# Performance work log

Hardware: AMD Instinct MI355X
Metric: run time of the kernel (lower is better)

Reference implementation:

```python
import jax, jax.numpy as jnp
import numpy as np

B, T, E, H = 4, 2048, 1024, 16
HS = E // H  # head_size = 64


def setup_inputs() -> dict:
    key = jax.random.key(0)
    ks = jax.random.split(key, 5)
    x = jax.random.normal(ks[0], (B, T, E), jnp.float32)
    scale = 0.02
    Wq = jax.random.normal(ks[1], (H, E, HS), jnp.float32) * scale
    Wk = jax.random.normal(ks[2], (H, E, HS), jnp.float32) * scale
    Wv = jax.random.normal(ks[3], (H, E, HS), jnp.float32) * scale
    Wo = jax.random.normal(ks[4], (E, E), jnp.float32) * scale
    bo = jnp.zeros((E,), jnp.float32)
    return {"x": x, "Wq": Wq, "Wk": Wk, "Wv": Wv, "Wo": Wo, "bo": bo}


def reference(x, Wq, Wk, Wv, Wo, bo):
    b, t, e = x.shape
    # per-head projections, batched over heads
    Q = jnp.einsum('bte,hed->bhtd', x, Wq)  # (B,H,T,HS)
    K = jnp.einsum('bte,hed->bhtd', x, Wk)
    V = jnp.einsum('bte,hed->bhtd', x, Wv)
    # faithful quirk 1: scale by sqrt(embd_size), not sqrt(head_size)
    scores = jnp.einsum('bhtd,bhsd->bhts', Q, K) / jnp.sqrt(jnp.float32(e))
    mask = jnp.tril(jnp.ones((t, t), dtype=bool))  # (T_q, T_k)
    scores = jnp.where(mask[None, None, :, :], scores, -jnp.inf)
    # faithful quirk 2: original softmaxes over dim=1 of (B,Tq,Tk) = the QUERY axis
    attn = jax.nn.softmax(scores, axis=2)
    out = jnp.einsum('bhts,bhsd->bhtd', attn, V)  # (B,H,T,HS)
    out = out.transpose(0, 2, 1, 3).reshape(b, t, e)  # concat heads -> (B,T,E)
    return out @ Wo + bo
```

## Files before the change

kernel.cpp:

```cpp
#include <hip/hip_runtime.h>
#include <stdint.h>

#define Bn 4
#define Tn 2048
#define En 1024
#define Hn 16
#define HSn 64
#define BHn (Bn*Hn)
#define NRn (Bn*Tn)

#define CEXP 0.0450840831f

typedef __attribute__((ext_vector_type(8))) short short8;
typedef __attribute__((ext_vector_type(4))) float f32x4;
typedef __attribute__((ext_vector_type(16))) float f32x16;
typedef __attribute__((ext_vector_type(4))) unsigned int uint4w;

__device__ __forceinline__ unsigned short f2b(float f){
  union { float f; unsigned int u; } c; c.f = f;
  unsigned int u = c.u + 0x7FFFu + ((c.u >> 16) & 1u);
  return (unsigned short)(u >> 16);
}
__device__ __forceinline__ float b2f(unsigned short s){
  union { unsigned int u; float f; } c; c.u = ((unsigned int)s) << 16;
  return c.f;
}
__device__ __forceinline__ unsigned int cvtpk(float lo, float hi){
  unsigned int r;
  asm("v_cvt_pk_bf16_f32 %0, %1, %2" : "=v"(r) : "v"(lo), "v"(hi));
  return r;
}
__device__ __forceinline__ f32x4 mfma16(short8 a, short8 b, f32x4 c){
  return __builtin_amdgcn_mfma_f32_16x16x32_bf16(a, b, c, 0, 0, 0);
}
__device__ __forceinline__ f32x16 mfma32(short8 a, short8 b, f32x16 c){
  return __builtin_amdgcn_mfma_f32_32x32x16_bf16(a, b, c, 0, 0, 0);
}
__device__ __forceinline__ void gl16(const void* g, void* s){
  __builtin_amdgcn_global_load_lds((const __attribute__((address_space(1))) unsigned int*)g,
                                   (__attribute__((address_space(3))) unsigned int*)s, 16, 0, 0);
}

__global__ void k_cvt_x(const float* __restrict__ x, unsigned short* __restrict__ xb){
  int i = (blockIdx.x * blockDim.x + threadIdx.x) * 8;
  float4 a = *(const float4*)(x + i);
  float4 b = *(const float4*)(x + i + 4);
  alignas(16) unsigned short o[8] = {f2b(a.x),f2b(a.y),f2b(a.z),f2b(a.w),
                                     f2b(b.x),f2b(b.y),f2b(b.z),f2b(b.w)};
  *(uint4w*)(xb + i) = *(const uint4w*)o;
}

__global__ void k_wT(const float* __restrict__ Wq, const float* __restrict__ Wk,
                     const float* __restrict__ Wv, const float* __restrict__ Wo,
                     unsigned short* __restrict__ Wt, unsigned short* __restrict__ Wot)
{
  __shared__ unsigned short Ls[64*80];
  const int tid = threadIdx.x;
  const int ey = blockIdx.x, jt = blockIdx.y;
  const int e0 = ey*64;
  const float* src; int R, c0; unsigned short* outp;
  if (jt < 48){
    int sel = jt >> 4, h = jt & 15;
    const float* W = (sel==0)?Wq:((sel==1)?Wk:Wv);
    src = W + h*(En*HSn); R = HSn; c0 = 0;
    outp = Wt + jt*64*En;
  } else {
    src = Wo; R = En; c0 = (jt-48)*64;
    outp = Wot + (jt-48)*64*En;
  }
  {
    const int e = tid >> 2, cq = (tid & 3)*16;
    const float* p = src + (e0 + e)*R + c0 + cq;
    float vv[16];
    *(float4*)&vv[0]  = *(const float4*)(p);
    *(float4*)&vv[4]  = *(const float4*)(p+4);
    *(float4*)&vv[8]  = *(const float4*)(p+8);
    *(float4*)&vv[12] = *(const float4*)(p+12);
#pragma unroll
    for (int i = 0; i < 16; i++) Ls[(cq+i)*80 + e] = f2b(vv[i]);
  }
  __syncthreads();
  {
    const int c8 = tid & 7, r = tid >> 3;
#pragma unroll
    for (int rr0 = 0; rr0 < 2; rr0++){
      int rr = r + rr0*32;
      *(uint4w*)(outp + rr*En + e0 + c8*8) = *(const uint4w*)&Ls[rr*80 + c8*8];
    }
  }
}

__global__ void __launch_bounds__(256, 2)
k_qkv(const unsigned short* __restrict__ xb,
      const unsigned short* __restrict__ Wt,
      unsigned short* __restrict__ Qb, unsigned short* __restrict__ Kb,
      unsigned short* __restrict__ Vt)
{
  __shared__ unsigned short As[2][128*64];
  __shared__ unsigned short Bs[2][128*64];
  const int tid = threadIdx.x, lane = tid & 63, w = tid >> 6;
  const int wr = w >> 1, wc = w & 1;
  const int mb = blockIdx.x, nb = blockIdx.y;
  const int n0 = nb*128;
  const int sel = n0 >> 10;
  const int nj0 = n0 & 1023;
  const int l15 = lane & 15, kc = lane >> 4;
  const int r8 = lane >> 3, c7 = lane & 7;

  const unsigned short* xbase = xb + (mb*128)*En;
  const unsigned short* wbase = Wt + n0*En;

  f32x4 acc[4][4];
#pragma unroll
  for (int i = 0; i < 4; i++)
#pragma unroll
    for (int j = 0; j < 4; j++) acc[i][j] = (f32x4){0.f,0.f,0.f,0.f};

  auto stage = [&](int buf, int k0){
#pragma unroll
    for (int i = 0; i < 4; i++){
      const int rb = w*32 + i*8;
      const int r = rb + r8;
      const int g = (c7 ^ r8) * 8;
      gl16(xbase + r*En + k0 + g, &As[buf][rb*64]);
      gl16(wbase + r*En + k0 + g, &Bs[buf][rb*64]);
    }
  };

  stage(0, 0);
  __syncthreads();

  for (int kt = 0; kt < 16; kt++){
    const int cur = kt & 1;
    if (kt < 15) stage(cur ^ 1, (kt + 1)*64);
    const unsigned short* Ac = &As[cur][0];
    const unsigned short* Bc = &Bs[cur][0];
#pragma unroll
    for (int ks = 0; ks < 2; ks++){
      short8 af[4], bf[4];
#pragma unroll
      for (int mf = 0; mf < 4; mf++){
        int ar = wr*64 + mf*16 + l15;
        af[mf] = *(const short8*)&Ac[ar*64 + (((ks*4 + kc) ^ (ar & 7))*8)];
      }
#pragma unroll
      for (int nf = 0; nf < 4; nf++){
        int br = wc*64 + nf*16 + l15;
        bf[nf] = *(const short8*)&Bc[br*64 + (((ks*4 + kc) ^ (br & 7))*8)];
      }
      __builtin_amdgcn_s_setprio(1);
#pragma unroll
      for (int mf = 0; mf < 4; mf++)
#pragma unroll
        for (int nf = 0; nf < 4; nf++)
          acc[mf][nf] = mfma16(af[mf], bf[nf], acc[mf][nf]);
      __builtin_amdgcn_s_setprio(0);
    }
    __syncthreads();
  }

  const int q4 = (lane >> 4)*4;
  const int bb = mb >> 4;
  const int tt0 = (mb*128) & 2047;

  if (sel == 2){
    unsigned short* tb = ((w < 2) ? &As[0][0] : &Bs[0][0]) + (w & 1)*8192;
#pragma unroll
    for (int nf = 0; nf < 4; nf++)
#pragma unroll
      for (int mf = 0; mf < 4; mf++){
        uint2 u;
        u.x = cvtpk(acc[mf][nf][0], acc[mf][nf][1]);
        u.y = cvtpk(acc[mf][nf][2], acc[mf][nf][3]);
        *(uint2*)&tb[(nf*16 + l15)*72 + mf*16 + q4] = u;
      }
    const int hh = (nj0 >> 6) + wc;
    unsigned short* vb = Vt + ((bb*Hn + hh)*HSn)*Tn + tt0 + wr*64;
#pragma unroll
    for (int i = 0; i < 8; i++){
      int rr = i*8 + r8;
      *(uint4w*)(vb + rr*Tn + c7*8) = *(const uint4w*)&tb[rr*72 + c7*8];
    }
  } else {
    unsigned short* Out = (sel == 1) ? Kb : Qb;
#pragma unroll
    for (int nf = 0; nf < 4; nf++){
      int jj = nj0 + wc*64 + nf*16 + l15;
      int hh = jj >> 6, dd = jj & 63;
#pragma unroll
      for (int mf = 0; mf < 4; mf++){
#pragma unroll
        for (int q = 0; q < 4; q++){
          int tt = tt0 + wr*64 + mf*16 + q4 + q;
          Out[((bb*Hn + hh)*Tn + tt)*HSn + dd] = f2b(acc[mf][nf][q]);
        }
      }
    }
  }
}

__global__ void k_colsum(const unsigned short* __restrict__ Qb,
                         const unsigned short* __restrict__ Kb,
                         float* __restrict__ Linv)
{
  __shared__ unsigned short Qs[2][128*64];
  __shared__ float Lred[64];
  const int bh = blockIdx.x, ipair = blockIdx.y;
  const int tid = threadIdx.x, lane = tid & 63, w = tid >> 6;
  const int l5 = lane >> 5, l31 = lane & 31;

  for (int ph = 0; ph < 2; ph++){
    const int sb = ph ? (31 - ipair) : ipair;
    const int s0 = sb * 64;

    short8 kf[2][4];
#pragma unroll
    for (int sf = 0; sf < 2; sf++){
      const unsigned short* kr = Kb + (bh*Tn + s0 + sf*32 + l31)*HSn + 8*l5;
#pragma unroll
      for (int ks = 0; ks < 4; ks++) kf[sf][ks] = *(const short8*)(kr + 16*ks);
    }

    float ls[2][16];
#pragma unroll
    for (int sf = 0; sf < 2; sf++)
#pragma unroll
      for (int r = 0; r < 16; r++) ls[sf][r] = 0.f;

    if (tid < 64) Lred[tid] = 0.f;

    const int t0s = (s0 >> 7) << 7;
    const int ntl = (Tn - t0s) >> 7;

    {
      const int c = lane & 7;
#pragma unroll
      for (int i = 0; i < 4; i++){
        int row = (w*4 + i)*8 + (lane >> 3);
        gl16(Qb + (bh*Tn + t0s + row)*HSn + ((c ^ (row & 7))*8), &Qs[0][(w*4 + i)*512]);
      }
    }
    asm volatile("s_waitcnt vmcnt(0)" ::: "memory");
    __syncthreads();

    for (int it = 0; it < ntl; it++){
      const int cur = it & 1;
      if (it + 1 < ntl){
        const int tn = t0s + (it + 1)*128;
        const int c = lane & 7;
#pragma unroll
        for (int i = 0; i < 4; i++){
          int row = (w*4 + i)*8 + (lane >> 3);
          gl16(Qb + (bh*Tn + tn + row)*HSn + ((c ^ (row & 7))*8), &Qs[cur^1][(w*4 + i)*512]);
        }
      }
      const int t0 = t0s + it*128;
      const int tw = t0 + 32*w;
      if (tw + 31 >= s0){
        f32x16 st[2];
#pragma unroll
        for (int sf = 0; sf < 2; sf++)
#pragma unroll
          for (int r = 0; r < 16; r++) st[sf][r] = 0.f;
        const int qrow = w*32 + l31;
        const unsigned short* Qc = &Qs[cur][qrow*64];
        const int sw = qrow & 7;
        __builtin_amdgcn_s_setprio(1);
#pragma unroll
        for (int ks = 0; ks < 4; ks++){
          short8 qb = *(const short8*)&Qc[((l5 + 2*ks) ^ sw)*8];
          st[0] = mfma32(kf[0][ks], qb, st[0]);
          st[1] = mfma32(kf[1][ks], qb, st[1]);
        }
        __builtin_amdgcn_s_setprio(0);
        const int tg = tw + l31;
        if (s0 + 63 <= tw){
#pragma unroll
          for (int sf = 0; sf < 2; sf++)
#pragma unroll
            for (int r = 0; r < 16; r++)
              ls[sf][r] += __builtin_amdgcn_exp2f(st[sf][r] * CEXP);
        } else {
#pragma unroll
          for (int sf = 0; sf < 2; sf++)
#pragma unroll
            for (int r = 0; r < 16; r++){
              int sg = s0 + 32*sf + (r & 3) + 8*(r >> 2) + 4*l5;
              float e = __builtin_amdgcn_exp2f(st[sf][r] * CEXP);
              ls[sf][r] += (tg >= sg) ? e : 0.f;
            }
        }
      }
      asm volatile("s_waitcnt vmcnt(0)" ::: "memory");
      __syncthreads();
    }

#pragma unroll
    for (int sf = 0; sf < 2; sf++)
#pragma unroll
      for (int r = 0; r < 16; r++){
        float v = ls[sf][r];
        v += __shfl_xor(v, 1);  v += __shfl_xor(v, 2);
        v += __shfl_xor(v, 4);  v += __shfl_xor(v, 8);
        v += __shfl_xor(v, 16);
        ls[sf][r] = v;
      }
    if (l31 == 0){
#pragma unroll
      for (int sf = 0; sf < 2; sf++)
#pragma unroll
        for (int r = 0; r < 16; r++){
          int sl = 32*sf + (r & 3) + 8*(r >> 2) + 4*l5;
          atomicAdd(&Lred[sl], ls[sf][r]);
        }
    }
    __syncthreads();
    if (tid < 64) Linv[bh*Tn + s0 + tid] = 1.0f / Lred[tid];
    if (ph == 0) __syncthreads();
  }
}

__global__ void k_vscale(unsigned short* __restrict__ Vt, const float* __restrict__ Linv){
  int i = (blockIdx.x * blockDim.x + threadIdx.x) * 8;
  int bh = i >> 17, t = i & 2047;
  short8 v = *(const short8*)(Vt + i);
  float4 L0 = *(const float4*)(Linv + bh*Tn + t);
  float4 L1 = *(const float4*)(Linv + bh*Tn + t + 4);
  unsigned int r0 = cvtpk(b2f((unsigned short)v[0])*L0.x, b2f((unsigned short)v[1])*L0.y);
  unsigned int r1 = cvtpk(b2f((unsigned short)v[2])*L0.z, b2f((unsigned short)v[3])*L0.w);
  unsigned int r2 = cvtpk(b2f((unsigned short)v[4])*L1.x, b2f((unsigned short)v[5])*L1.y);
  unsigned int r3 = cvtpk(b2f((unsigned short)v[6])*L1.z, b2f((unsigned short)v[7])*L1.w);
  uint4w o; o[0]=r0; o[1]=r1; o[2]=r2; o[3]=r3;
  *(uint4w*)(Vt + i) = o;
}

__global__ void __launch_bounds__(256, 4)
k_attn(const unsigned short* __restrict__ Qb,
       const unsigned short* __restrict__ Kb,
       const unsigned short* __restrict__ Vlt,
       unsigned short* __restrict__ Att)
{
  __shared__ unsigned short Ks[2][64*64];
  __shared__ unsigned short Vs[2][64*64];
  const int bh = blockIdx.x;
  const int tb = 15 - blockIdx.y;
  const int t0 = tb * 128;
  const int tid = threadIdx.x, lane = tid & 63, w = tid >> 6;
  const int l5 = lane >> 5, l31 = lane & 31;
  const int c7 = lane & 7, r8 = lane >> 3;
  const int tbase = t0 + w*32;
  const int nt = 2*tb + 2;

  short8 qf[4];
  {
    const unsigned short* qr = Qb + (bh*Tn + tbase + l31)*HSn + 8*l5;
#pragma unroll
    for (int ks = 0; ks < 4; ks++) qf[ks] = *(const short8*)(qr + 16*ks);
  }

  f32x16 oacc[2];
#pragma unroll
  for (int df = 0; df < 2; df++)
#pragma unroll
    for (int r = 0; r < 16; r++) oacc[df][r] = 0.f;

#pragma unroll
  for (int i = 0; i < 2; i++){
    int row = (w*2 + i)*8 + r8;
    gl16(Kb  + (bh*Tn + row)*HSn + ((c7 ^ (row & 7))*8), &Ks[0][(w*2 + i)*512]);
    gl16(Vlt + (bh*HSn + row)*Tn + ((c7 ^ (row & 7))*8), &Vs[0][(w*2 + i)*512]);
  }
  asm volatile("s_waitcnt vmcnt(0)" ::: "memory");
  __syncthreads();

  for (int it = 0; it < nt; it++){
    const int cur = it & 1;
    if (it + 1 < nt){
      const int sn = (it + 1)*64;
#pragma unroll
      for (int i = 0; i < 2; i++){
        int row = (w*2 + i)*8 + r8;
        gl16(Kb  + (bh*Tn + sn + row)*HSn + ((c7 ^ (row & 7))*8), &Ks[cur^1][(w*2 + i)*512]);
        gl16(Vlt + (bh*HSn + row)*Tn + sn + ((c7 ^ (row & 7))*8), &Vs[cur^1][(w*2 + i)*512]);
      }
    }
    const int s0 = it * 64;
    if (s0 <= tbase + 31){
      const unsigned short* Kc = &Ks[cur][0];
      f32x16 st[2];
#pragma unroll
      for (int sf = 0; sf < 2; sf++)
#pragma unroll
        for (int r = 0; r < 16; r++) st[sf][r] = 0.f;
      __builtin_amdgcn_s_setprio(1);
#pragma unroll
      for (int ks = 0; ks < 4; ks++){
#pragma unroll
        for (int sf = 0; sf < 2; sf++){
          int row = sf*32 + l31;
          short8 ka = *(const short8*)&Kc[row*64 + (((l5 + 2*ks) ^ (row & 7))*8)];
          st[sf] = mfma32(ka, qf[ks], st[sf]);
        }
      }
      __builtin_amdgcn_s_setprio(0);

      const int tg = tbase + l31;
      const bool interior = (s0 + 63 <= tbase);
#pragma unroll
      for (int sf = 0; sf < 2; sf++){
#pragma unroll
        for (int r = 0; r < 16; r++){
          float e = __builtin_amdgcn_exp2f(st[sf][r] * CEXP);
          if (!interior){
            int sg = s0 + 32*sf + (r & 3) + 8*(r >> 2) + 4*l5;
            e = (tg >= sg) ? e : 0.f;
          }
          st[sf][r] = e;
        }
      }

      short8 pb[4];
#pragma unroll
      for (int sf = 0; sf < 2; sf++){
#pragma unroll
        for (int q = 0; q < 2; q++){
          unsigned int ax = cvtpk(st[sf][8*q+0], st[sf][8*q+1]);
          unsigned int ay = cvtpk(st[sf][8*q+2], st[sf][8*q+3]);
          unsigned int bx = cvtpk(st[sf][8*q+4], st[sf][8*q+5]);
          unsigned int by = cvtpk(st[sf][8*q+6], st[sf][8*q+7]);
          asm("v_permlane32_swap_b32 %0, %1" : "+v"(ax), "+v"(bx));
          asm("v_permlane32_swap_b32 %0, %1" : "+v"(ay), "+v"(by));
          union { unsigned int u[4]; short8 s; } pk;
          pk.u[0] = ax; pk.u[1] = ay; pk.u[2] = bx; pk.u[3] = by;
          pb[sf*2 + q] = pk.s;
        }
      }

      const unsigned short* Vc = &Vs[cur][0];
      __builtin_amdgcn_s_setprio(1);
#pragma unroll
      for (int ks = 0; ks < 4; ks++){
#pragma unroll
        for (int df = 0; df < 2; df++){
          int row = df*32 + l31;
          short8 va = *(const short8*)&Vc[row*64 + (((l5 + 2*ks) ^ (row & 7))*8)];
          oacc[df] = mfma32(va, pb[ks], oacc[df]);
        }
      }
      __builtin_amdgcn_s_setprio(0);
    }
    asm volatile("s_waitcnt vmcnt(0)" ::: "memory");
    __syncthreads();
  }

  {
    const int tg = tbase + l31;
    unsigned short* ob = Att + (bh*Tn + tg)*HSn;
#pragma unroll
    for (int df = 0; df < 2; df++)
#pragma unroll
      for (int r2 = 0; r2 < 4; r2++){
        uint2 u;
        u.x = cvtpk(oacc[df][r2*4+0], oacc[df][r2*4+1]);
        u.y = cvtpk(oacc[df][r2*4+2], oacc[df][r2*4+3]);
        *(uint2*)&ob[32*df + 8*r2 + 4*l5] = u;
      }
  }
}

__global__ void __launch_bounds__(256, 2)
k_oproj(const unsigned short* __restrict__ Att,
        const unsigned short* __restrict__ Wot,
        const float* __restrict__ bo, float* __restrict__ out)
{
  __shared__ unsigned short As[2][128*64];
  __shared__ unsigned short Bs[2][128*64];
  const int tid = threadIdx.x, lane = tid & 63, w = tid >> 6;
  const int wr = w >> 1, wc = w & 1;
  const int mb = blockIdx.x, nb = blockIdx.y;
  const int n0 = nb*128;
  const int l15 = lane & 15, kc = lane >> 4;
  const int r8 = lane >> 3, c7 = lane & 7;
  const int bb = mb >> 4;
  const int t0 = (mb*128) & 2047;

  f32x4 acc[4][4];
#pragma unroll
  for (int i = 0; i < 4; i++)
#pragma unroll
    for (int j = 0; j < 4; j++) acc[i][j] = (f32x4){0.f,0.f,0.f,0.f};

  const unsigned short* wbase = Wot + n0*En;

  auto stage = [&](int buf, int k0){
    const int hh = k0 >> 6;
    const unsigned short* abase = Att + ((bb*Hn + hh)*Tn + t0)*HSn;
#pragma unroll
    for (int i = 0; i < 4; i++){
      const int rb = w*32 + i*8;
      const int r = rb + r8;
      const int g = (c7 ^ r8) * 8;
      gl16(abase + r*HSn + g, &As[buf][rb*64]);
      gl16(wbase + r*En + k0 + g, &Bs[buf][rb*64]);
    }
  };

  stage(0, 0);
  __syncthreads();

  for (int kt = 0; kt < 16; kt++){
    const int cur = kt & 1;
    if (kt < 15) stage(cur ^ 1, (kt + 1)*64);
    const unsigned short* Ac = &As[cur][0];
    const unsigned short* Bc = &Bs[cur][0];
#pragma unroll
    for (int ks = 0; ks < 2; ks++){
      short8 af[4], bf[4];
#pragma unroll
      for (int mf = 0; mf < 4; mf++){
        int ar = wr*64 + mf*16 + l15;
        af[mf] = *(const short8*)&Ac[ar*64 + (((ks*4 + kc) ^ (ar & 7))*8)];
      }
#pragma unroll
      for (int nf = 0; nf < 4; nf++){
        int br = wc*64 + nf*16 + l15;
        bf[nf] = *(const short8*)&Bc[br*64 + (((ks*4 + kc) ^ (br & 7))*8)];
      }
      __builtin_amdgcn_s_setprio(1);
#pragma unroll
      for (int mf = 0; mf < 4; mf++)
#pragma unroll
        for (int nf = 0; nf < 4; nf++)
          acc[mf][nf] = mfma16(af[mf], bf[nf], acc[mf][nf]);
      __builtin_amdgcn_s_setprio(0);
    }
    __syncthreads();
  }

  const int q4 = (lane >> 4)*4;
#pragma unroll
  for (int nf = 0; nf < 4; nf++){
    int j = n0 + wc*64 + nf*16 + l15;
    float bias = bo[j];
#pragma unroll
    for (int mf = 0; mf < 4; mf++){
#pragma unroll
      for (int q = 0; q < 4; q++){
        int rr = mb*128 + wr*64 + mf*16 + q4 + q;
        out[rr*En + j] = acc[mf][nf][q] + bias;
      }
    }
  }
}

extern "C" void kernel_launch(void* const* d_in, const int* in_sizes, int n_in,
                              void* d_out, int out_size, void* d_ws, size_t ws_size,
                              hipStream_t stream)
{
  (void)in_sizes; (void)n_in; (void)out_size; (void)ws_size;
  const float* x  = (const float*)d_in[0];
  const float* Wq = (const float*)d_in[1];
  const float* Wk = (const float*)d_in[2];
  const float* Wv = (const float*)d_in[3];
  const float* Wo = (const float*)d_in[4];
  const float* bo = (const float*)d_in[5];
  float* out = (float*)d_out;

  uint8_t* w = (uint8_t*)d_ws;
  unsigned short* Qb  = (unsigned short*)(w);
  unsigned short* Kb  = (unsigned short*)(w + (16u << 20));
  unsigned short* Vt  = (unsigned short*)(w + (32u << 20));
  unsigned short* xb  = (unsigned short*)(w + (48u << 20));
  unsigned short* Att = (unsigned short*)(w + (48u << 20));
  unsigned short* Wt  = (unsigned short*)(w + (64u << 20));
  unsigned short* Wot = (unsigned short*)(w + (70u << 20));
  float* Linv         = (float*)(w + (72u << 20));

  hipLaunchKernelGGL(k_cvt_x,  dim3(4096),    dim3(256), 0, stream, x, xb);
  hipLaunchKernelGGL(k_wT,     dim3(16, 64),  dim3(256), 0, stream, Wq, Wk, Wv, Wo, Wt, Wot);
  hipLaunchKernelGGL(k_qkv,    dim3(64, 24),  dim3(256), 0, stream, xb, Wt, Qb, Kb, Vt);
  hipLaunchKernelGGL(k_colsum, dim3(64, 16),  dim3(256), 0, stream, Qb, Kb, Linv);
  hipLaunchKernelGGL(k_vscale, dim3(4096),    dim3(256), 0, stream, Vt, Linv);
  hipLaunchKernelGGL(k_attn,   dim3(64, 16),  dim3(256), 0, stream, Qb, Kb, Vt, Att);
  hipLaunchKernelGGL(k_oproj,  dim3(64, 8),   dim3(256), 0, stream, Att, Wot, bo, out);
}
```

Baseline: 209.9 us.

## Prefetch two tiles ahead with partial vmcnt waits in all kernels

Restructures the double-buffered global_load_lds pipelines in the QKV GEMM, the column-sum pass, the attention kernel and the output GEMM. Each now issues loads two tiles ahead and waits with a partial vmcnt instead of draining all loads every iteration, so loads stay in flight across compute. The cost is an extra barrier per iteration and fragile wait-count bookkeeping. With only two buffers, a buffer is refilled right after its compute finishes, so the lookahead depends on the barrier placement being correct.

```diff
diff --git a/kernel.cpp b/kernel.cpp
--- a/kernel.cpp
+++ b/kernel.cpp
@@ -40,6 +40,9 @@
   __builtin_amdgcn_global_load_lds((const __attribute__((address_space(1))) unsigned int*)g,
                                    (__attribute__((address_space(3))) unsigned int*)s, 16, 0, 0);
 }
+#define FENCE()    asm volatile("" ::: "memory")
+#define WAITV(N)   asm volatile("s_waitcnt vmcnt(" #N ")" ::: "memory")
+#define SBAR()     __builtin_amdgcn_s_barrier()
 
 __global__ void k_cvt_x(const float* __restrict__ x, unsigned short* __restrict__ xb){
   int i = (blockIdx.x * blockDim.x + threadIdx.x) * 8;
@@ -126,13 +129,7 @@
       gl16(wbase + r*En + k0 + g, &Bs[buf][rb*64]);
     }
   };
-
-  stage(0, 0);
-  __syncthreads();
-
-  for (int kt = 0; kt < 16; kt++){
-    const int cur = kt & 1;
-    if (kt < 15) stage(cur ^ 1, (kt + 1)*64);
+  auto compute = [&](int cur){
     const unsigned short* Ac = &As[cur][0];
     const unsigned short* Bc = &Bs[cur][0];
 #pragma unroll
@@ -156,8 +153,24 @@
           acc[mf][nf] = mfma16(af[mf], bf[nf], acc[mf][nf]);
       __builtin_amdgcn_s_setprio(0);
     }
-    __syncthreads();
-  }
+  };
+
+  stage(0, 0);
+  stage(1, 64);
+  WAITV(8); SBAR();
+
+  for (int kt = 0; kt < 16; kt++){
+    const int cur = kt & 1;
+    compute(cur);
+    FENCE(); SBAR();
+    if (kt < 14){
+      stage(cur, (kt + 2)*64);
+      WAITV(8); SBAR();
+    } else if (kt == 14){
+      WAITV(0); SBAR();
+    }
+  }
+  __syncthreads();
 
   const int q4 = (lane >> 4)*4;
   const int bb = mb >> 4;
@@ -232,28 +245,22 @@
     const int t0s = (s0 >> 7) << 7;
     const int ntl = (Tn - t0s) >> 7;
 
-    {
+    auto stageQ = [&](int buf, int tg0){
       const int c = lane & 7;
 #pragma unroll
       for (int i = 0; i < 4; i++){
         int row = (w*4 + i)*8 + (lane >> 3);
-        gl16(Qb + (bh*Tn + t0s + row)*HSn + ((c ^ (row & 7))*8), &Qs[0][(w*4 + i)*512]);
-      }
-    }
-    asm volatile("s_waitcnt vmcnt(0)" ::: "memory");
-    __syncthreads();
+        gl16(Qb + (bh*Tn + tg0 + row)*HSn + ((c ^ (row & 7))*8), &Qs[buf][(w*4 + i)*512]);
+      }
+    };
+
+    stageQ(0, t0s);
+    if (ntl > 1){ stageQ(1, t0s + 128); WAITV(4); }
+    else        { WAITV(0); }
+    SBAR();
 
     for (int it = 0; it < ntl; it++){
       const int cur = it & 1;
-      if (it + 1 < ntl){
-        const int tn = t0s + (it + 1)*128;
-        const int c = lane & 7;
-#pragma unroll
-        for (int i = 0; i < 4; i++){
-          int row = (w*4 + i)*8 + (lane >> 3);
-          gl16(Qb + (bh*Tn + tn + row)*HSn + ((c ^ (row & 7))*8), &Qs[cur^1][(w*4 + i)*512]);
-        }
-      }
       const int t0 = t0s + it*128;
       const int tw = t0 + 32*w;
       if (tw + 31 >= s0){
@@ -291,8 +298,13 @@
             }
         }
       }
-      asm volatile("s_waitcnt vmcnt(0)" ::: "memory");
-      __syncthreads();
+      FENCE(); SBAR();
+      if (it + 2 < ntl){
+        stageQ(cur, t0s + (it + 2)*128);
+        WAITV(4); SBAR();
+      } else if (it + 2 == ntl){
+        WAITV(0); SBAR();
+      }
     }
 
 #pragma unroll
@@ -364,26 +376,21 @@
 #pragma unroll
     for (int r = 0; r < 16; r++) oacc[df][r] = 0.f;
 
-#pragma unroll
-  for (int i = 0; i < 2; i++){
-    int row = (w*2 + i)*8 + r8;
-    gl16(Kb  + (bh*Tn + row)*HSn + ((c7 ^ (row & 7))*8), &Ks[0][(w*2 + i)*512]);
-    gl16(Vlt + (bh*HSn + row)*Tn + ((c7 ^ (row & 7))*8), &Vs[0][(w*2 + i)*512]);
-  }
-  asm volatile("s_waitcnt vmcnt(0)" ::: "memory");
-  __syncthreads();
+  auto stageKV = [&](int buf, int sn){
+#pragma unroll
+    for (int i = 0; i < 2; i++){
+      int row = (w*2 + i)*8 + r8;
+      gl16(Kb  + (bh*Tn + sn + row)*HSn + ((c7 ^ (row & 7))*8), &Ks[buf][(w*2 + i)*512]);
+      gl16(Vlt + (bh*HSn + row)*Tn + sn + ((c7 ^ (row & 7))*8), &Vs[buf][(w*2 + i)*512]);
+    }
+  };
+
+  stageKV(0, 0);
+  stageKV(1, 64);
+  WAITV(4); SBAR();
 
   for (int it = 0; it < nt; it++){
     const int cur = it & 1;
-    if (it + 1 < nt){
-      const int sn = (it + 1)*64;
-#pragma unroll
-      for (int i = 0; i < 2; i++){
-        int row = (w*2 + i)*8 + r8;
-        gl16(Kb  + (bh*Tn + sn + row)*HSn + ((c7 ^ (row & 7))*8), &Ks[cur^1][(w*2 + i)*512]);
-        gl16(Vlt + (bh*HSn + row)*Tn + sn + ((c7 ^ (row & 7))*8), &Vs[cur^1][(w*2 + i)*512]);
-      }
-    }
     const int s0 = it * 64;
     if (s0 <= tbase + 31){
       const unsigned short* Kc = &Ks[cur][0];
@@ -449,8 +456,13 @@
       }
       __builtin_amdgcn_s_setprio(0);
     }
-    asm volatile("s_waitcnt vmcnt(0)" ::: "memory");
-    __syncthreads();
+    FENCE(); SBAR();
+    if (it + 2 < nt){
+      stageKV(cur, (it + 2)*64);
+      WAITV(4); SBAR();
+    } else if (it + 2 == nt){
+      WAITV(0); SBAR();
+    }
   }
 
   {
@@ -504,13 +516,7 @@
       gl16(wbase + r*En + k0 + g, &Bs[buf][rb*64]);
     }
   };
-
-  stage(0, 0);
-  __syncthreads();
-
-  for (int kt = 0; kt < 16; kt++){
-    const int cur = kt & 1;
-    if (kt < 15) stage(cur ^ 1, (kt + 1)*64);
+  auto compute = [&](int cur){
     const unsigned short* Ac = &As[cur][0];
     const unsigned short* Bc = &Bs[cur][0];
 #pragma unroll
@@ -534,7 +540,22 @@
           acc[mf][nf] = mfma16(af[mf], bf[nf], acc[mf][nf]);
       __builtin_amdgcn_s_setprio(0);
     }
-    __syncthreads();
+  };
+
+  stage(0, 0);
+  stage(1, 64);
+  WAITV(8); SBAR();
+
+  for (int kt = 0; kt < 16; kt++){
+    const int cur = kt & 1;
+    compute(cur);
+    FENCE(); SBAR();
+    if (kt < 14){
+      stage(cur, (kt + 2)*64);
+      WAITV(8); SBAR();
+    } else if (kt == 14){
+      WAITV(0); SBAR();
+    }
   }
 
   const int q4 = (lane >> 4)*4;
```

Result: no change. 209.1 us (-0.4%).
